# Optimization experiments

Measured on AMD Instinct MI355X. Metric: run time of the kernel, lower is better.

The kernel has to match this reference:

```python
import jax, jax.numpy as jnp
import numpy as np

B, HQ, HK, S, D, HID, BS = 2, 32, 8, 8192, 128, 128, 16
NB = S // BS  # 512 pooled blocks


def rotate_half(x):
    h = x.shape[-1] // 2
    return jnp.concatenate([-x[..., h:], x[..., :h]], axis=-1)


def pool_cat(x):
    # avg + max pooling over block_size along the sequence dim, concat on feature dim
    b, h, s, d = x.shape
    xb = x.reshape(b, h, s // BS, BS, d)
    return jnp.concatenate([xb.mean(axis=3), xb.max(axis=3)], axis=-1)  # [b,h,NB,2d]


def setup_inputs() -> dict:
    key = jax.random.key(0)
    k0, k1, k2, k3 = jax.random.split(key, 4)
    q = jax.random.normal(k0, (B, HQ, S, D), jnp.float32)
    k = jax.random.normal(k1, (B, HK, S, D), jnp.float32)
    wq = jax.random.normal(k2, (HQ, 2 * D, HID), jnp.float32) / np.float32(np.sqrt(2 * D))
    wk = jax.random.normal(k3, (HK, 2 * D, HID), jnp.float32) / np.float32(np.sqrt(2 * D))
    # causal block mask
    mask = jnp.broadcast_to(jnp.tril(jnp.ones((NB, NB), bool))[None, None], (B, 1, NB, NB))
    # RoPE tables over pooled positions
    pos = jnp.arange(NB, dtype=jnp.float32)
    inv_freq = 1.0 / (10000.0 ** (jnp.arange(0, HID, 2, dtype=jnp.float32) / HID))
    freqs = pos[:, None] * inv_freq[None, :]              # [NB, HID/2]
    emb = jnp.concatenate([freqs, freqs], axis=-1)        # [NB, HID]
    cos = jnp.broadcast_to(jnp.cos(emb)[None], (B, NB, HID))
    sin = jnp.broadcast_to(jnp.sin(emb)[None], (B, NB, HID))
    return {"q": q, "k": k, "attention_mask": mask, "cos": cos, "sin": sin, "wq": wq, "wk": wk}


def reference(q, k, attention_mask, cos, sin, wq, wk):
    # pooled multi-head linear projections
    qh = jnp.einsum('bhnc,hcd->bhnd', pool_cat(q), wq)   # [B,HQ,NB,HID]
    kh = jnp.einsum('bhnc,hcd->bhnd', pool_cat(k), wk)   # [B,HK,NB,HID]
    # RoPE (unsqueeze_dim=1)
    c, s = cos[:, None], sin[:, None]
    qh = qh * c + rotate_half(qh) * s
    kh = kh * c + rotate_half(kh) * s
    # GQA: repeat kv heads
    kh = jnp.repeat(kh, HQ // HK, axis=1)                # [B,HQ,NB,HID]
    attn = jnp.einsum('bhqd,bhkd->bhqk', qh, kh) / jnp.sqrt(jnp.float32(HID))
    attn = jnp.where(attention_mask, attn, jnp.float32(-1e9))
    return jax.nn.softmax(attn, axis=-1)
```

## Files before the change

kernel.cpp:

```cpp
#include <hip/hip_runtime.h>

namespace {
constexpr int BB  = 2;
constexpr int HQ  = 32;
constexpr int HK  = 8;
constexpr int S   = 8192;
constexpr int D   = 128;
constexpr int HID = 128;
constexpr int BS  = 16;
constexpr int NB  = 512;
constexpr int C2D = 256;
constexpr int RW  = 256;
}

typedef __attribute__((ext_vector_type(8))) short short8;
typedef __attribute__((ext_vector_type(4))) float f32x4;

__device__ inline unsigned short f2bf(float f) {
  unsigned u = __builtin_bit_cast(unsigned, f);
  unsigned r = u + 0x7fff + ((u >> 16) & 1);
  return (unsigned short)(r >> 16);
}
__device__ inline float bf2f(unsigned short s) {
  unsigned u = ((unsigned)s) << 16;
  return __builtin_bit_cast(float, u);
}

__global__ __launch_bounds__(256) void pool_gemm_rope_kernel(
    const float* __restrict__ qx, const float* __restrict__ kx,
    const float* __restrict__ wqp, const float* __restrict__ wkp,
    const float* __restrict__ cosp, const float* __restrict__ sinp,
    unsigned short* __restrict__ qhb, unsigned short* __restrict__ khb)
{
  constexpr int PST = 260;
  constexpr int RST = 132;
  __shared__ float smem[32 * PST];

  const int t  = threadIdx.x;
  const int n0 = blockIdx.x * 32;
  const int hy = blockIdx.y;
  const int b  = blockIdx.z;

  const float* x; const float* w; unsigned short* o; int H; int h; bool isq;
  if (hy < HQ) { x = qx; w = wqp; o = qhb; H = HQ; h = hy; isq = true; }
  else         { x = kx; w = wkp; o = khb; H = HK; h = hy - HQ; isq = false; }

  const float* xb = x + (((size_t)b * H + h) * S + (size_t)n0 * BS) * D;
  for (int it = t; it < 32 * 32; it += 256) {
    const int m = it >> 5, d4 = it & 31;
    const float4* p = (const float4*)(xb + (size_t)m * BS * D) + d4;
    float4 v = p[0];
    float sx = v.x, sy = v.y, sz = v.z, sw = v.w;
    float mx = v.x, my = v.y, mz = v.z, mw = v.w;
#pragma unroll
    for (int i = 1; i < BS; ++i) {
      v = p[i * (D / 4)];
      sx += v.x; sy += v.y; sz += v.z; sw += v.w;
      mx = fmaxf(mx, v.x); my = fmaxf(my, v.y);
      mz = fmaxf(mz, v.z); mw = fmaxf(mw, v.w);
    }
    const float inv16 = 1.0f / 16.0f;
    *(float4*)&smem[m * PST + 4 * d4] =
        make_float4(sx * inv16, sy * inv16, sz * inv16, sw * inv16);
    *(float4*)&smem[m * PST + 128 + 4 * d4] = make_float4(mx, my, mz, mw);
  }
  __syncthreads();

  const int dt = t & 31, mt = t >> 5;
  const int d0 = dt * 4, m0 = mt * 4;
  const float* wb = w + (size_t)h * C2D * HID;
  float4 acc[4];
#pragma unroll
  for (int i = 0; i < 4; ++i) acc[i] = make_float4(0.f, 0.f, 0.f, 0.f);

  for (int c = 0; c < C2D; c += 4) {
    const float4 w0 = *(const float4*)(wb + (size_t)(c + 0) * HID + d0);
    const float4 w1 = *(const float4*)(wb + (size_t)(c + 1) * HID + d0);
    const float4 w2 = *(const float4*)(wb + (size_t)(c + 2) * HID + d0);
    const float4 w3 = *(const float4*)(wb + (size_t)(c + 3) * HID + d0);
#pragma unroll
    for (int i = 0; i < 4; ++i) {
      const float4 pv = *(const float4*)&smem[(m0 + i) * PST + c];
      acc[i].x += pv.x * w0.x + pv.y * w1.x + pv.z * w2.x + pv.w * w3.x;
      acc[i].y += pv.x * w0.y + pv.y * w1.y + pv.z * w2.y + pv.w * w3.y;
      acc[i].z += pv.x * w0.z + pv.y * w1.z + pv.z * w2.z + pv.w * w3.z;
      acc[i].w += pv.x * w0.w + pv.y * w1.w + pv.z * w2.w + pv.w * w3.w;
    }
  }
  __syncthreads();

#pragma unroll
  for (int i = 0; i < 4; ++i)
    *(float4*)&smem[(m0 + i) * RST + d0] = acc[i];
  __syncthreads();

  const float sgn = (d0 < 64) ? -1.0f : 1.0f;
  const float qscale = isq ? 0.08838834764831843f : 1.0f;
#pragma unroll
  for (int i = 0; i < 4; ++i) {
    const int n = n0 + m0 + i;
    const float4 cv = *(const float4*)(cosp + ((size_t)b * NB + n) * HID + d0);
    const float4 sv = *(const float4*)(sinp + ((size_t)b * NB + n) * HID + d0);
    const float4 pr = *(const float4*)&smem[(m0 + i) * RST + (d0 ^ 64)];
    float ov[4];
    ov[0] = (acc[i].x * cv.x + sgn * pr.x * sv.x) * qscale;
    ov[1] = (acc[i].y * cv.y + sgn * pr.y * sv.y) * qscale;
    ov[2] = (acc[i].z * cv.z + sgn * pr.z * sv.z) * qscale;
    ov[3] = (acc[i].w * cv.w + sgn * pr.w * sv.w) * qscale;
    ushort4 hi, lo;
    hi.x = f2bf(ov[0]); lo.x = f2bf(ov[0] - bf2f(hi.x));
    hi.y = f2bf(ov[1]); lo.y = f2bf(ov[1] - bf2f(hi.y));
    hi.z = f2bf(ov[2]); lo.z = f2bf(ov[2] - bf2f(hi.z));
    hi.w = f2bf(ov[3]); lo.w = f2bf(ov[3] - bf2f(hi.w));
    unsigned short* orow = o + (((size_t)b * H + h) * NB + n) * RW + d0;
    *(ushort4*)orow = hi;
    *(ushort4*)(orow + 128) = lo;
  }
}

__global__ __launch_bounds__(256) void attn_kernel(
    const unsigned short* __restrict__ qhb,
    const unsigned short* __restrict__ khb,
    float* __restrict__ out)
{
  __shared__ float rs_lds[16];

  const int t = threadIdx.x;
  const int w = t >> 6;
  const int lane = t & 63;
  const int col = lane & 15;
  const int quad = lane >> 4;
  const int x = blockIdx.x;
  const int h = blockIdx.y;
  const int b = blockIdx.z;

  const unsigned short* qbase = qhb + (((size_t)b * HQ + h) * NB) * RW;
  const unsigned short* kbase = khb + (((size_t)b * HK + (h >> 2)) * NB) * RW;
  float* obase = out + (((size_t)b * HQ + h) * NB) * (size_t)NB;

  for (int ph = 0; ph < 2; ++ph) {
    const int strip = ph ? (31 - x) : x;

    __syncthreads();
    if (t < 16) rs_lds[t] = 0.f;
    __syncthreads();

    const unsigned short* qrow = qbase + (size_t)(strip * 16 + col) * RW + quad * 8;
    short8 qf[8];
#pragma unroll
    for (int f = 0; f < 4; ++f) {
      qf[f]     = *(const short8*)(qrow + f * 32);
      qf[4 + f] = *(const short8*)(qrow + f * 32 + 128);
    }

    const unsigned short* krow = kbase + (size_t)col * RW + quad * 8;
    const int n = (w <= strip) ? ((strip - w) >> 2) + 1 : 0;

    f32x4 pbuf[8];
    float rs[4] = {0.f, 0.f, 0.f, 0.f};

#pragma unroll
    for (int ti = 0; ti < 8; ++ti) {
      if (ti < n) {
        const int k16 = w + 4 * ti;
        const unsigned short* kr = krow + (size_t)k16 * 16 * RW;
        short8 kf[8];
#pragma unroll
        for (int f = 0; f < 4; ++f) {
          kf[f]     = *(const short8*)(kr + f * 32);
          kf[4 + f] = *(const short8*)(kr + f * 32 + 128);
        }
        f32x4 acc = {0.f, 0.f, 0.f, 0.f};
#pragma unroll
        for (int f = 0; f < 4; ++f) {
          acc = __builtin_amdgcn_mfma_f32_16x16x32_bf16(qf[f],     kf[f],     acc, 0, 0, 0);
          acc = __builtin_amdgcn_mfma_f32_16x16x32_bf16(qf[f],     kf[4 + f], acc, 0, 0, 0);
          acc = __builtin_amdgcn_mfma_f32_16x16x32_bf16(qf[4 + f], kf[f],     acc, 0, 0, 0);
        }
        const bool diag = (k16 == strip);
        f32x4 p;
#pragma unroll
        for (int r = 0; r < 4; ++r) {
          float v = __expf(acc[r]);
          if (diag && col > quad * 4 + r) v = 0.f;
          p[r] = v;
          rs[r] += v;
        }
        pbuf[ti] = p;
      }
    }

#pragma unroll
    for (int r = 0; r < 4; ++r) {
      float v = rs[r];
      v += __shfl_xor(v, 1, 64);
      v += __shfl_xor(v, 2, 64);
      v += __shfl_xor(v, 4, 64);
      v += __shfl_xor(v, 8, 64);
      if (col == 0) atomicAdd(&rs_lds[quad * 4 + r], v);
    }

    {
      const int r = t & 15;
      const float4 z = make_float4(0.f, 0.f, 0.f, 0.f);
      for (int c4 = (strip + 1) * 4 + (t >> 4); c4 < 128; c4 += 16)
        *(float4*)(obase + (size_t)(strip * 16 + r) * NB + 4 * c4) = z;
    }

    __syncthreads();

    float inv[4];
#pragma unroll
    for (int r = 0; r < 4; ++r) inv[r] = 1.0f / rs_lds[quad * 4 + r];

#pragma unroll
    for (int ti = 0; ti < 8; ++ti) {
      if (ti < n) {
        const int k16 = w + 4 * ti;
#pragma unroll
        for (int r = 0; r < 4; ++r)
          obase[(size_t)(strip * 16 + quad * 4 + r) * NB + k16 * 16 + col] =
              pbuf[ti][r] * inv[r];
      }
    }
  }
}

extern "C" void kernel_launch(void* const* d_in, const int* in_sizes, int n_in,
                              void* d_out, int out_size, void* d_ws, size_t ws_size,
                              hipStream_t stream)
{
  const float* q    = (const float*)d_in[0];
  const float* k    = (const float*)d_in[1];
  const float* cosp = (const float*)d_in[3];
  const float* sinp = (const float*)d_in[4];
  const float* wq   = (const float*)d_in[5];
  const float* wk   = (const float*)d_in[6];
  float* out = (float*)d_out;

  unsigned short* qhb = (unsigned short*)d_ws;
  unsigned short* khb = qhb + (size_t)BB * HQ * NB * RW;

  hipLaunchKernelGGL(pool_gemm_rope_kernel, dim3(NB / 32, HQ + HK, BB), dim3(256),
                     0, stream, q, k, wq, wk, cosp, sinp, qhb, khb);
  hipLaunchKernelGGL(attn_kernel, dim3(16, HQ, BB), dim3(256),
                     0, stream, qhb, khb, out);
}
```

Measured before the change: 487.2 us.

## Move pooled projection GEMM onto bf16x3 MFMA with pre-transposed split weights

Adds a weight-prep kernel that transposes each head's projection weights and splits them into bf16 hi/lo halves. The pooling stage now stores pooled features as bf16 hi/lo in LDS, and the projection runs as three-term split-bf16 MFMA instead of scalar FP32 FMAs. This targets the FP32 ALU cost of the projection GEMM, at the price of an extra kernel launch, extra workspace and slightly different rounding. The weight prep runs on every call.

```diff
diff --git a/kernel.cpp b/kernel.cpp
--- a/kernel.cpp
+++ b/kernel.cpp
@@ -11,6 +11,7 @@
 constexpr int NB  = 512;
 constexpr int C2D = 256;
 constexpr int RW  = 256;
+constexpr int WTR = 512;
 }
 
 typedef __attribute__((ext_vector_type(8))) short short8;
@@ -26,24 +27,60 @@
   return __builtin_bit_cast(float, u);
 }
 
+__global__ __launch_bounds__(256) void wprep_kernel(
+    const float* __restrict__ wq, const float* __restrict__ wk,
+    unsigned short* __restrict__ wT)
+{
+  __shared__ float ts[32 * 33];
+  const int t  = threadIdx.x;
+  const int kc = blockIdx.x;
+  const int hy = blockIdx.y;
+  const float* w = (hy < HQ) ? (wq + (size_t)hy * C2D * HID)
+                             : (wk + (size_t)(hy - HQ) * C2D * HID);
+  for (int nc = 0; nc < 4; ++nc) {
+    __syncthreads();
+    {
+      const int r = t >> 3, c4 = t & 7;
+      *(float4*)&ts[r * 33 + 4 * c4] =
+          *(const float4*)(w + (size_t)(kc * 32 + r) * HID + nc * 32 + 4 * c4);
+    }
+    __syncthreads();
+    {
+      const int n = t >> 3, g = t & 7;
+      const int cb = 8 * (g & 3);
+      short8 v;
+#pragma unroll
+      for (int j = 0; j < 8; ++j) {
+        const float f = ts[(cb + j) * 33 + n];
+        const unsigned short h = f2bf(f);
+        v[j] = (short)((g < 4) ? h : f2bf(f - bf2f(h)));
+      }
+      unsigned short* dst = wT + ((size_t)hy * HID + nc * 32 + n) * WTR +
+                            ((g < 4) ? 0 : 256) + kc * 32 + cb;
+      *(short8*)dst = v;
+    }
+  }
+}
+
 __global__ __launch_bounds__(256) void pool_gemm_rope_kernel(
     const float* __restrict__ qx, const float* __restrict__ kx,
-    const float* __restrict__ wqp, const float* __restrict__ wkp,
+    const unsigned short* __restrict__ wT,
     const float* __restrict__ cosp, const float* __restrict__ sinp,
     unsigned short* __restrict__ qhb, unsigned short* __restrict__ khb)
 {
-  constexpr int PST = 260;
-  constexpr int RST = 132;
-  __shared__ float smem[32 * PST];
+  constexpr int AST = 520;
+  constexpr int CST = 132;
+  __shared__ unsigned short As[32 * AST];
+  float* Cs = (float*)As;
 
   const int t  = threadIdx.x;
   const int n0 = blockIdx.x * 32;
   const int hy = blockIdx.y;
   const int b  = blockIdx.z;
 
-  const float* x; const float* w; unsigned short* o; int H; int h; bool isq;
-  if (hy < HQ) { x = qx; w = wqp; o = qhb; H = HQ; h = hy; isq = true; }
-  else         { x = kx; w = wkp; o = khb; H = HK; h = hy - HQ; isq = false; }
+  const float* x; unsigned short* o; int H; int h; bool isq;
+  if (hy < HQ) { x = qx; o = qhb; H = HQ; h = hy; isq = true; }
+  else         { x = kx; o = khb; H = HK; h = hy - HQ; isq = false; }
 
   const float* xb = x + (((size_t)b * H + h) * S + (size_t)n0 * BS) * D;
   for (int it = t; it < 32 * 32; it += 256) {
@@ -60,40 +97,64 @@
       mz = fmaxf(mz, v.z); mw = fmaxf(mw, v.w);
     }
     const float inv16 = 1.0f / 16.0f;
-    *(float4*)&smem[m * PST + 4 * d4] =
-        make_float4(sx * inv16, sy * inv16, sz * inv16, sw * inv16);
-    *(float4*)&smem[m * PST + 128 + 4 * d4] = make_float4(mx, my, mz, mw);
-  }
+    float mn[4] = {sx * inv16, sy * inv16, sz * inv16, sw * inv16};
+    float mv[4] = {mx, my, mz, mw};
+    ushort4 mh, ml, xh, xl;
+    mh.x = f2bf(mn[0]); ml.x = f2bf(mn[0] - bf2f(mh.x));
+    mh.y = f2bf(mn[1]); ml.y = f2bf(mn[1] - bf2f(mh.y));
+    mh.z = f2bf(mn[2]); ml.z = f2bf(mn[2] - bf2f(mh.z));
+    mh.w = f2bf(mn[3]); ml.w = f2bf(mn[3] - bf2f(mh.w));
+    xh.x = f2bf(mv[0]); xl.x = f2bf(mv[0] - bf2f(xh.x));
+    xh.y = f2bf(mv[1]); xl.y = f2bf(mv[1] - bf2f(xh.y));
+    xh.z = f2bf(mv[2]); xl.z = f2bf(mv[2] - bf2f(xh.z));
+    xh.w = f2bf(mv[3]); xl.w = f2bf(mv[3] - bf2f(xh.w));
+    unsigned short* row = &As[m * AST];
+    *(ushort4*)(row + 4 * d4)       = mh;
+    *(ushort4*)(row + 256 + 4 * d4) = ml;
+    *(ushort4*)(row + 128 + 4 * d4) = xh;
+    *(ushort4*)(row + 384 + 4 * d4) = xl;
+  }
+  __syncthreads();
+
+  const int w    = t >> 6;
+  const int lane = t & 63;
+  const int col  = lane & 15;
+  const int quad = lane >> 4;
+  const int mtile = w & 1;
+  const int nbase = (w >> 1) * 64;
+
+  const unsigned short* arow = &As[(size_t)(mtile * 16 + col) * AST + quad * 8];
+  const unsigned short* bp = wT + ((size_t)hy * HID + nbase + col) * WTR + quad * 8;
+
+  f32x4 acc[4];
+#pragma unroll
+  for (int i = 0; i < 4; ++i) acc[i] = (f32x4){0.f, 0.f, 0.f, 0.f};
+
+#pragma unroll
+  for (int ks = 0; ks < 8; ++ks) {
+    const short8 ahi = *(const short8*)(arow + ks * 32);
+    const short8 alo = *(const short8*)(arow + 256 + ks * 32);
+#pragma unroll
+    for (int nt = 0; nt < 4; ++nt) {
+      const short8 bhi = *(const short8*)(bp + (size_t)nt * 16 * WTR + ks * 32);
+      const short8 blo = *(const short8*)(bp + (size_t)nt * 16 * WTR + 256 + ks * 32);
+      acc[nt] = __builtin_amdgcn_mfma_f32_16x16x32_bf16(ahi, bhi, acc[nt], 0, 0, 0);
+      acc[nt] = __builtin_amdgcn_mfma_f32_16x16x32_bf16(ahi, blo, acc[nt], 0, 0, 0);
+      acc[nt] = __builtin_amdgcn_mfma_f32_16x16x32_bf16(alo, bhi, acc[nt], 0, 0, 0);
+    }
+  }
+  __syncthreads();
+
+#pragma unroll
+  for (int nt = 0; nt < 4; ++nt)
+#pragma unroll
+    for (int r = 0; r < 4; ++r)
+      Cs[(size_t)(mtile * 16 + quad * 4 + r) * CST + nbase + nt * 16 + col] =
+          acc[nt][r];
   __syncthreads();
 
   const int dt = t & 31, mt = t >> 5;
   const int d0 = dt * 4, m0 = mt * 4;
-  const float* wb = w + (size_t)h * C2D * HID;
-  float4 acc[4];
-#pragma unroll
-  for (int i = 0; i < 4; ++i) acc[i] = make_float4(0.f, 0.f, 0.f, 0.f);
-
-  for (int c = 0; c < C2D; c += 4) {
-    const float4 w0 = *(const float4*)(wb + (size_t)(c + 0) * HID + d0);
-    const float4 w1 = *(const float4*)(wb + (size_t)(c + 1) * HID + d0);
-    const float4 w2 = *(const float4*)(wb + (size_t)(c + 2) * HID + d0);
-    const float4 w3 = *(const float4*)(wb + (size_t)(c + 3) * HID + d0);
-#pragma unroll
-    for (int i = 0; i < 4; ++i) {
-      const float4 pv = *(const float4*)&smem[(m0 + i) * PST + c];
-      acc[i].x += pv.x * w0.x + pv.y * w1.x + pv.z * w2.x + pv.w * w3.x;
-      acc[i].y += pv.x * w0.y + pv.y * w1.y + pv.z * w2.y + pv.w * w3.y;
-      acc[i].z += pv.x * w0.z + pv.y * w1.z + pv.z * w2.z + pv.w * w3.z;
-      acc[i].w += pv.x * w0.w + pv.y * w1.w + pv.z * w2.w + pv.w * w3.w;
-    }
-  }
-  __syncthreads();
-
-#pragma unroll
-  for (int i = 0; i < 4; ++i)
-    *(float4*)&smem[(m0 + i) * RST + d0] = acc[i];
-  __syncthreads();
-
   const float sgn = (d0 < 64) ? -1.0f : 1.0f;
   const float qscale = isq ? 0.08838834764831843f : 1.0f;
 #pragma unroll
@@ -101,12 +162,13 @@
     const int n = n0 + m0 + i;
     const float4 cv = *(const float4*)(cosp + ((size_t)b * NB + n) * HID + d0);
     const float4 sv = *(const float4*)(sinp + ((size_t)b * NB + n) * HID + d0);
-    const float4 pr = *(const float4*)&smem[(m0 + i) * RST + (d0 ^ 64)];
+    const float4 cur = *(const float4*)&Cs[(m0 + i) * CST + d0];
+    const float4 pr  = *(const float4*)&Cs[(m0 + i) * CST + (d0 ^ 64)];
     float ov[4];
-    ov[0] = (acc[i].x * cv.x + sgn * pr.x * sv.x) * qscale;
-    ov[1] = (acc[i].y * cv.y + sgn * pr.y * sv.y) * qscale;
-    ov[2] = (acc[i].z * cv.z + sgn * pr.z * sv.z) * qscale;
-    ov[3] = (acc[i].w * cv.w + sgn * pr.w * sv.w) * qscale;
+    ov[0] = (cur.x * cv.x + sgn * pr.x * sv.x) * qscale;
+    ov[1] = (cur.y * cv.y + sgn * pr.y * sv.y) * qscale;
+    ov[2] = (cur.z * cv.z + sgn * pr.z * sv.z) * qscale;
+    ov[3] = (cur.w * cv.w + sgn * pr.w * sv.w) * qscale;
     ushort4 hi, lo;
     hi.x = f2bf(ov[0]); lo.x = f2bf(ov[0] - bf2f(hi.x));
     hi.y = f2bf(ov[1]); lo.y = f2bf(ov[1] - bf2f(hi.y));
@@ -240,9 +302,12 @@
 
   unsigned short* qhb = (unsigned short*)d_ws;
   unsigned short* khb = qhb + (size_t)BB * HQ * NB * RW;
-
+  unsigned short* wTp = khb + (size_t)BB * HK * NB * RW;
+
+  hipLaunchKernelGGL(wprep_kernel, dim3(8, HQ + HK), dim3(256),
+                     0, stream, wq, wk, wTp);
   hipLaunchKernelGGL(pool_gemm_rope_kernel, dim3(NB / 32, HQ + HK, BB), dim3(256),
-                     0, stream, q, k, wq, wk, cosp, sinp, qhb, khb);
+                     0, stream, q, k, wTp, cosp, sinp, qhb, khb);
   hipLaunchKernelGGL(attn_kernel, dim3(16, HQ, BB), dim3(256),
                      0, stream, qhb, khb, out);
 }
```

Result: no change. 480.3 us (-1.4%).
